# Performance work log

Hardware: AMD Instinct MI355X
Metric: run time of the kernel (lower is better)

Reference implementation:

```python
import jax, jax.numpy as jnp
import numpy as np

B, H, W, C = 2, 128, 128, 128
K = 3            # window_size
NB = K * K       # neighbor_count = 9
RP = 8           # relative_position_dim
HID = 128        # edge hidden = max(256//2, 128)
EIN = 3 * C + RP # edge_input_dim = 392
CLIP = 3.0
GEPS = 1e-06     # gate_eps
LNE = 1e-05      # LayerNorm eps


def _ln(x, g, b):
    m = x.mean(-1, keepdims=True)
    v = ((x - m) ** 2).mean(-1, keepdims=True)
    return (x - m) * jax.lax.rsqrt(v + LNE) * g + b


def setup_inputs() -> dict:
    key = jax.random.key(0)
    ks = jax.random.split(key, 12)
    f32 = jnp.float32
    inp = {
        'tokens': jax.random.normal(ks[0], (B, H, W, C), dtype=f32),
        'ln1_g': jnp.ones((C,), f32), 'ln1_b': jnp.zeros((C,), f32),
        'ln2_g': jnp.ones((C,), f32), 'ln2_b': jnp.zeros((C,), f32),
        'rel_pos': 0.02 * jax.random.normal(ks[1], (NB, RP), dtype=f32),
        'dW1': 0.01 * jax.random.normal(ks[2], (EIN, HID), dtype=f32),
        'db1': jnp.zeros((HID,), f32),
        'dW2': 0.01 * jax.random.normal(ks[3], (HID, 1), dtype=f32),
        'db2': jnp.zeros((1,), f32),
        'rW1': 0.01 * jax.random.normal(ks[4], (EIN, HID), dtype=f32),
        'rb1': jnp.zeros((HID,), f32),
        'rW2': 0.01 * jax.random.normal(ks[5], (HID, 1), dtype=f32),
        'rb2': jnp.zeros((1,), f32),
        'vW': 0.01 * jax.random.normal(ks[6], (C, C), dtype=f32),
        'vb': jnp.zeros((C,), f32),
        'oW': 0.01 * jax.random.normal(ks[7], (C, C), dtype=f32),
        'ob': jnp.zeros((C,), f32),
        'eml_gamma': jnp.asarray(0.1, f32),
        'eml_lam': jnp.asarray(1.0, f32),
        'eml_bias': jnp.asarray(-0.3, f32),
    }
    return inp


def _edge_mlp(x, W1, b1, W2, b2):
    h = jax.nn.gelu(jnp.einsum('blnd,dh->blnh', x, W1) + b1, approximate=False)
    return jnp.einsum('blnh,ho->blno', h, W2) + b2


def _forward(tokens, ln1_g, ln1_b, ln2_g, ln2_b, rel_pos, dW1, db1, dW2, db2,
             rW1, rb1, rW2, rb2, vW, vb, oW, ob, eml_gamma, eml_lam, eml_bias,
             warmup_eta=1.0):
    Bh, Hh, Wh, Ch = tokens.shape
    L = Hh * Wh
    normalized = _ln(tokens, ln1_g, ln1_b)
    flat = normalized.reshape(Bh, L, Ch)
    # Unfold(kernel=3, padding=1): gather 9 shifted views, then replicate torch's
    # reshape of the (C, 9)-ordered channel axis into (9, C).
    pad = jnp.pad(normalized, ((0, 0), (1, 1), (1, 1), (0, 0)))
    shifts = [pad[:, i:i + Hh, j:j + Wh, :] for i in range(K) for j in range(K)]
    nbhd = jnp.stack(shifts, axis=-1)                       # [B,H,W,C,9]
    nbhd = nbhd.reshape(Bh, L, Ch * NB).reshape(Bh, L, NB, Ch)  # torch reshape semantics
    center = jnp.broadcast_to(flat[:, :, None, :], nbhd.shape)
    rel = jnp.broadcast_to(rel_pos[None, None], (Bh, L, NB, rel_pos.shape[-1]))
    edge_features = jnp.concatenate([center, nbhd, center - nbhd, rel], axis=-1)
    drive = _edge_mlp(edge_features, dW1, db1, dW2, db2)[..., 0]        # [B,L,9]
    resistance = _edge_mlp(edge_features, rW1, rb1, rW2, rb2)[..., 0]   # [B,L,9]
    # EML unit (Ohm's-law style gate): clamp(eta*gamma*drive/(lambda*softplus(R)+eps)+bias)
    energy = jnp.clip(
        warmup_eta * (eml_gamma * drive) / (eml_lam * jax.nn.softplus(resistance) + GEPS)
        + eml_bias, -CLIP, CLIP)
    gate = jax.nn.sigmoid(energy)                                        # [B,L,9]
    values = jnp.einsum('blnc,cd->blnd', nbhd, vW) + vb                  # [B,L,9,C]
    gate_mass = jnp.maximum(gate.sum(axis=2), GEPS)                      # [B,L]
    message = jnp.einsum('bln,blnc->blc', gate, values) / gate_mass[..., None]
    update = (jnp.einsum('blc,cd->bld', message, oW) + ob).reshape(Bh, Hh, Wh, Ch)
    output = _ln(tokens + update, ln2_g, ln2_b)  # dropout is identity at eval
    return output


def reference(tokens, ln1_g, ln1_b, ln2_g, ln2_b, rel_pos, dW1, db1, dW2, db2,
              rW1, rb1, rW2, rb2, vW, vb, oW, ob, eml_gamma, eml_lam, eml_bias):
    return _forward(tokens, ln1_g, ln1_b, ln2_g, ln2_b, rel_pos, dW1, db1, dW2, db2,
                    rW1, rb1, rW2, rb2, vW, vb, oW, ob, eml_gamma, eml_lam, eml_bias)
```

## Files before the change

### kernel.cpp

```cpp
#include <hip/hip_runtime.h>


#define USHORT unsigned short
#define AW 152

typedef __attribute__((ext_vector_type(8)))  __bf16 v8bf;
typedef __attribute__((ext_vector_type(8)))  USHORT v8u;
typedef __attribute__((ext_vector_type(16))) float  v16f;

__device__ __forceinline__ USHORT f2bf(float f) {
    unsigned v; __builtin_memcpy(&v, &f, 4);
    v += 0x7FFFu + ((v >> 16) & 1u);
    return (USHORT)(v >> 16);
}

template <int C>
__device__ __forceinline__ float dpps(float x) {
    return __int_as_float(
        __builtin_amdgcn_update_dpp(0, __float_as_int(x), C, 0xf, 0xf, true));
}
__device__ __forceinline__ float red32half(float x) {
    x += dpps<0x111>(x);
    x += dpps<0x112>(x);
    x += dpps<0x114>(x);
    x += dpps<0x118>(x);
    x += dpps<0x142>(x);
    return x;
}
__device__ __forceinline__ float red64(float x) {
    x = red32half(x);
    x += dpps<0x143>(x);
    return x;
}
__device__ __forceinline__ float bcast63(float x) {
    return __int_as_float(__builtin_amdgcn_readlane(__float_as_int(x), 63));
}

__global__ __launch_bounds__(256) void k_setup(
    const float* __restrict__ tok, const float* __restrict__ ln1g,
    const float* __restrict__ ln1b,
    const float* __restrict__ dW1, const float* __restrict__ db1,
    const float* __restrict__ rW1, const float* __restrict__ rb1,
    const float* __restrict__ rel, const float* __restrict__ dW2,
    const float* __restrict__ rW2, const float* __restrict__ vW,
    const float* __restrict__ vb,  const float* __restrict__ oW,
    USHORT* __restrict__ norm,
    USHORT* __restrict__ WnTg, USHORT* __restrict__ WcTg, USHORT* __restrict__ VTg,
    float* __restrict__ preg, float* __restrict__ vboWg, float* __restrict__ w2g)
{
    const int blk = blockIdx.x, t = threadIdx.x;
    if (blk >= 354) {
        const int p = (blk - 354) * 4 + (t >> 6);
        const int lane = t & 63;
        const float2 x = ((const float2*)(tok + (size_t)p * 128))[lane];
        float s = x.x + x.y;
        for (int m = 1; m < 64; m <<= 1) s += __shfl_xor(s, m);
        const float mean = s * (1.f / 128.f);
        const float d0 = x.x - mean, d1 = x.y - mean;
        float q = d0 * d0 + d1 * d1;
        for (int m = 1; m < 64; m <<= 1) q += __shfl_xor(q, m);
        const float rstd = rsqrtf(q * (1.f / 128.f) + 1e-5f);
        const float2 gg = ((const float2*)ln1g)[lane], bb = ((const float2*)ln1b)[lane];
        ((unsigned*)norm)[(size_t)p * 64 + lane] =
            (unsigned)f2bf(d0 * rstd * gg.x + bb.x) |
            ((unsigned)f2bf(d1 * rstd * gg.y + bb.y) << 16);
        return;
    }
    if (blk < 72) {
        int idx = blk * 256 + t;
        int n = ((idx >> 4) * 7282) >> 16;
        int k = idx - n * 144;
        int r = k >> 4, tt = k & 15, c2 = r + 9 * tt;
        float acc = 0.f;
        if (c2 < 128)
            for (int j = 0; j < 128; ++j) acc += vW[c2 * 128 + j] * oW[j * 128 + n];
        VTg[idx] = f2bf(acc);
    } else if (blk < 216) {
        int idx = (blk - 72) * 256 + t;
        int n = ((idx >> 4) * 7282) >> 16;
        int k = idx - n * 144;
        int r = k >> 4, tt = k & 15, c2 = r + 9 * tt;
        int col = n & 127;
        const float* W = (n < 128) ? dW1 : rW1;
        float val = 0.f;
        if (c2 < 128) val = W[(128 + c2) * 128 + col] - W[(256 + c2) * 128 + col];
        WnTg[idx] = f2bf(val);
    } else if (blk < 344) {
        int idx = (blk - 216) * 256 + t;
        int n = idx >> 7, c = idx & 127, col = n & 127;
        const float* W = (n < 128) ? dW1 : rW1;
        WcTg[idx] = f2bf(W[c * 128 + col] + W[(256 + c) * 128 + col]);
    } else if (blk < 353) {
        int n2 = blk - 344; int h = t;
        float acc;
        if (h < 128) {
            acc = db1[h];
            for (int r = 0; r < 8; ++r) acc += rel[n2 * 8 + r] * dW1[(384 + r) * 128 + h];
        } else {
            int hh = h - 128;
            acc = rb1[hh];
            for (int r = 0; r < 8; ++r) acc += rel[n2 * 8 + r] * rW1[(384 + r) * 128 + hh];
        }
        preg[n2 * 256 + h] = acc;
    } else {
        if (t < 128) {
            float acc = 0.f;
            for (int j = 0; j < 128; ++j) acc += vb[j] * oW[j * 128 + t];
            vboWg[t] = acc;
            w2g[t] = dW2[t];
            w2g[128 + t] = rW2[t];
        }
    }
}

__device__ __forceinline__ void gather_load(
    uint2 (&pf)[9], const USHORT* __restrict__ nb,
    int n2, int y, int bI, int tid)
{
    const int x = tid >> 2, q = tid & 3;
    #pragma unroll
    for (int r = 0; r < 9; ++r) {
        int u = 2 * n2 + r;
        int n = (u >= 18) ? (u - 18) : ((u >= 9) ? (u - 9) : u);
        int v = n2 * 128 + r;
        int c0 = (v * 7282) >> 16;
        int dyq = (n * 22) >> 6;
        int dx = n - 3 * dyq - 1;
        int dy = dyq - 1;
        int sy = y + dy, sx = x + dx;
        bool ok = ((unsigned)sy < 128u) && ((unsigned)sx < 128u);
        int e0 = (c0 & ~1) + 4 * q;
        size_t gidx = ((size_t)((bI * 128 + (ok ? sy : 0)) * 128 + (ok ? sx : 0))) * 128 + e0;
        const unsigned* gp = (const unsigned*)nb + (gidx >> 1);
        unsigned dw0 = gp[0], dw1 = gp[1];
        pf[r].x = ok ? dw0 : 0u;
        pf[r].y = ok ? dw1 : 0u;
    }
}

__device__ __forceinline__ void gather_store(
    USHORT* __restrict__ Adst, uint2 (&pf)[9], int n2, int tid)
{
    const int x = tid >> 2, q = tid & 3;
    #pragma unroll
    for (int r = 0; r < 9; ++r) {
        int v = n2 * 128 + r;
        int c0 = (v * 7282) >> 16;
        unsigned dw0 = pf[r].x, dw1 = pf[r].y;
        unsigned nxt = (unsigned)__shfl_down((int)dw0, 1);
        unsigned o0, o1;
        if (c0 & 1) { o0 = (dw0 >> 16) | (dw1 << 16); o1 = (dw1 >> 16) | (nxt << 16); }
        else        { o0 = dw0;                       o1 = dw1; }
        pf[r].x = o0; pf[r].y = o1;
        *(uint2*)(Adst + x * AW + 16 * r + 4 * q) = make_uint2(o0, o1);
    }
}

__global__ __launch_bounds__(512, 2) void k_edge(
    const float* __restrict__ tok, const float* __restrict__ ln2g,
    const float* __restrict__ ln2b, const USHORT* __restrict__ nb,
    const USHORT* __restrict__ WnTg, const USHORT* __restrict__ WcTg,
    const USHORT* __restrict__ VTg, const float* __restrict__ preg,
    const float* __restrict__ vboWg, const float* __restrict__ w2g,
    const float* __restrict__ db2p, const float* __restrict__ rb2p,
    const float* __restrict__ gmp, const float* __restrict__ lmp,
    const float* __restrict__ bip, const float* __restrict__ obp,
    float* __restrict__ out)
{
    extern __shared__ char smem[];
    USHORT* Wsh  = (USHORT*)smem;
    USHORT* Ash0 = (USHORT*)(smem + 77824);
    USHORT* Ash1 = (USHORT*)(smem + 116736);
    float*  w2L  = (float*)(smem + 155648);
    float*  dP   = (float*)(smem + 156672);
    float*  rP   = (float*)(smem + 158720);
    float*  sgL  = (float*)(smem + 160768);
    float*  updF = (float*)smem;

    const int tid = threadIdx.x;
    const int lane = tid & 63, wave = tid >> 6, hi = lane >> 5, l31 = lane & 31;
    const int mw = wave & 1, nw = wave >> 1;
    const int blk = blockIdx.x;
    const int bI = blk >> 7;
    const int y = ((blk & 7) << 4) | ((blk >> 3) & 15);
    const int p0 = (bI * 128 + y) * 128;

    for (int i = tid; i < 4096; i += 512) {
        int n = i >> 4, kv = i & 15;
        *(v8u*)(Wsh + n * AW + kv * 8) = *(const v8u*)(WcTg + n * 128 + kv * 8);
    }
    for (int i = tid; i < 2048; i += 512) {
        int x = i >> 4, kv = i & 15;
        *(v8u*)(Ash0 + x * AW + kv * 8) = *(const v8u*)(nb + (size_t)(p0 + x) * 128 + kv * 8);
    }
    if (tid < 256) w2L[tid] = w2g[tid];
    __syncthreads();

    v16f cp[2][2];
    #pragma unroll
    for (int a = 0; a < 2; ++a)
        for (int b = 0; b < 2; ++b)
            for (int e = 0; e < 16; ++e) cp[a][b][e] = 0.f;
    #pragma unroll
    for (int ks = 0; ks < 8; ++ks) {
        v8bf af0 = *(const v8bf*)(Ash0 + (mw * 64 + l31) * AW + ks * 16 + hi * 8);
        v8bf af1 = *(const v8bf*)(Ash0 + (mw * 64 + 32 + l31) * AW + ks * 16 + hi * 8);
        v8bf bf0 = *(const v8bf*)(Wsh + (nw * 64 + l31) * AW + ks * 16 + hi * 8);
        v8bf bf1 = *(const v8bf*)(Wsh + (nw * 64 + 32 + l31) * AW + ks * 16 + hi * 8);
        cp[0][0] = __builtin_amdgcn_mfma_f32_32x32x16_bf16(af0, bf0, cp[0][0], 0, 0, 0);
        cp[0][1] = __builtin_amdgcn_mfma_f32_32x32x16_bf16(af0, bf1, cp[0][1], 0, 0, 0);
        cp[1][0] = __builtin_amdgcn_mfma_f32_32x32x16_bf16(af1, bf0, cp[1][0], 0, 0, 0);
        cp[1][1] = __builtin_amdgcn_mfma_f32_32x32x16_bf16(af1, bf1, cp[1][1], 0, 0, 0);
    }
    __syncthreads();

    for (int i = tid; i < 4608; i += 512) {
        int n = (i * 3641) >> 16;
        int kv = i - n * 18;
        *(v8u*)(Wsh + n * AW + kv * 8) = *(const v8u*)(WnTg + n * 144 + kv * 8);
    }
    uint2 pfc[9];
    gather_load(pfc, nb, 0, y, bI, tid);
    gather_store(Ash0, pfc, 0, tid);

    const float gmv = gmp[0], lmv = lmp[0], biv = bip[0];
    const float db2v = db2p[0], rb2v = rb2p[0];
    const float wv0 = w2L[nw * 64 + l31];
    const float wv1 = w2L[nw * 64 + 32 + l31];

    float G[36];
    #pragma unroll
    for (int j = 0; j < 36; ++j) G[j] = 0.f;
    float sg = 0.f;
    const int grow = tid >> 2, gq = tid & 3;

    const int w32g = grow & 31;
    const int gslot = (((grow >> 6) * 2 + ((grow >> 5) & 1)) * 2 + ((w32g >> 2) & 1)) * 16
                      + ((w32g & 3) | (((w32g >> 3) & 3) << 2));

    float* sumHalf = ((nw < 2) ? dP : rP) + (nw & 1) * 128;

    __syncthreads();

    for (int n2 = 0; n2 < 9; ++n2) {
        const int par = n2 & 1;
        USHORT* Acur = par ? Ash1 : Ash0;
        USHORT* Anxt = par ? Ash0 : Ash1;
        const float pv0 = preg[n2 * 256 + nw * 64 + l31];
        const float pv1 = preg[n2 * 256 + nw * 64 + 32 + l31];

        uint2 raw[9];
        if (n2 < 8) gather_load(raw, nb, n2 + 1, y, bI, tid);

        v16f acc[2][2];
        #pragma unroll
        for (int a = 0; a < 2; ++a)
            for (int b = 0; b < 2; ++b) acc[a][b] = cp[a][b];
        #pragma unroll
        for (int ks = 0; ks < 9; ++ks) {
            v8bf af0 = *(const v8bf*)(Acur + (mw * 64 + l31) * AW + ks * 16 + hi * 8);
            v8bf af1 = *(const v8bf*)(Acur + (mw * 64 + 32 + l31) * AW + ks * 16 + hi * 8);
            v8bf bf0 = *(const v8bf*)(Wsh + (nw * 64 + l31) * AW + ks * 16 + hi * 8);
            v8bf bf1 = *(const v8bf*)(Wsh + (nw * 64 + 32 + l31) * AW + ks * 16 + hi * 8);
            acc[0][0] = __builtin_amdgcn_mfma_f32_32x32x16_bf16(af0, bf0, acc[0][0], 0, 0, 0);
            acc[0][1] = __builtin_amdgcn_mfma_f32_32x32x16_bf16(af0, bf1, acc[0][1], 0, 0, 0);
            acc[1][0] = __builtin_amdgcn_mfma_f32_32x32x16_bf16(af1, bf0, acc[1][0], 0, 0, 0);
            acc[1][1] = __builtin_amdgcn_mfma_f32_32x32x16_bf16(af1, bf1, acc[1][1], 0, 0, 0);
        }
        #pragma unroll
        for (int mt = 0; mt < 2; ++mt) {
            float part[16];
            #pragma unroll
            for (int rr = 0; rr < 16; ++rr) {
                float h0 = acc[mt][0][rr] + pv0;
                float h1 = acc[mt][1][rr] + pv1;
                float s0 = __builtin_amdgcn_rcpf(1.f + __expf(-1.702f * h0));
                float s1 = __builtin_amdgcn_rcpf(1.f + __expf(-1.702f * h1));
                part[rr] = h0 * s0 * wv0 + h1 * s1 * wv1;
            }
            #pragma unroll
            for (int rr = 0; rr < 16; ++rr) part[rr] = red32half(part[rr]);
            if (l31 == 31) {
                float* t0 = sumHalf + par * 256 + ((mw * 2 + mt) * 2 + hi) * 16;
                *(float4*)(t0 +  0) = make_float4(part[0],  part[1],  part[2],  part[3]);
                *(float4*)(t0 +  4) = make_float4(part[4],  part[5],  part[6],  part[7]);
                *(float4*)(t0 +  8) = make_float4(part[8],  part[9],  part[10], part[11]);
                *(float4*)(t0 + 12) = make_float4(part[12], part[13], part[14], part[15]);
            }
        }
        if (n2 < 8) gather_store(Anxt, raw, n2 + 1, tid);
        __syncthreads();

        {
            const int pb = par * 256;
            float d  = dP[pb + gslot] + dP[pb + 128 + gslot] + db2v;
            float rv = rP[pb + gslot] + rP[pb + 128 + gslot] + rb2v;
            float sp = fmaxf(rv, 0.f) + log1pf(__expf(-fabsf(rv)));
            float e = gmv * d / (lmv * sp + 1e-6f) + biv;
            e = fminf(fmaxf(e, -3.f), 3.f);
            float gt = 1.f / (1.f + __expf(-e));
            sg += gt;
            #pragma unroll
            for (int r = 0; r < 9; ++r) {
                unsigned o0 = pfc[r].x, o1 = pfc[r].y;
                G[4 * r + 0] += gt * __int_as_float((int)(o0 << 16));
                G[4 * r + 1] += gt * __int_as_float((int)(o0 & 0xFFFF0000u));
                G[4 * r + 2] += gt * __int_as_float((int)(o1 << 16));
                G[4 * r + 3] += gt * __int_as_float((int)(o1 & 0xFFFF0000u));
            }
        }
        if (n2 < 8) {
            #pragma unroll
            for (int r = 0; r < 9; ++r) pfc[r] = raw[r];
        }
    }

    {
        USHORT* dst = Ash0 + grow * AW + 4 * gq;
        #pragma unroll
        for (int r = 0; r < 9; ++r) {
            unsigned lo  = (unsigned)f2bf(G[4 * r + 0]) | ((unsigned)f2bf(G[4 * r + 1]) << 16);
            unsigned hi2 = (unsigned)f2bf(G[4 * r + 2]) | ((unsigned)f2bf(G[4 * r + 3]) << 16);
            *(uint2*)(dst + 16 * r) = make_uint2(lo, hi2);
        }
    }
    for (int i = tid; i < 2304; i += 512) {
        int n = (i * 3641) >> 16;
        int kv = i - n * 18;
        *(v8u*)(Ash1 + n * AW + kv * 8) = *(const v8u*)(VTg + n * 144 + kv * 8);
    }
    if (gq == 0) sgL[grow] = sg;
    __syncthreads();

    v16f P[2];
    #pragma unroll
    for (int a = 0; a < 2; ++a)
        for (int e = 0; e < 16; ++e) P[a][e] = 0.f;
    #pragma unroll
    for (int ks = 0; ks < 9; ++ks) {
        v8bf af0 = *(const v8bf*)(Ash0 + (mw * 64 + l31) * AW + ks * 16 + hi * 8);
        v8bf af1 = *(const v8bf*)(Ash0 + (mw * 64 + 32 + l31) * AW + ks * 16 + hi * 8);
        v8bf vf  = *(const v8bf*)(Ash1 + (nw * 32 + l31) * AW + ks * 16 + hi * 8);
        P[0] = __builtin_amdgcn_mfma_f32_32x32x16_bf16(af0, vf, P[0], 0, 0, 0);
        P[1] = __builtin_amdgcn_mfma_f32_32x32x16_bf16(af1, vf, P[1], 0, 0, 0);
    }

    {
        const int colc = nw * 32 + l31;
        const float vbw = vboWg[colc], obv = obp[colc];
        #pragma unroll
        for (int mt = 0; mt < 2; ++mt) {
            const int base = mw * 64 + mt * 32 + 4 * hi;
            const float4* sq = (const float4*)&sgL[base];
            float4 sa = sq[0], sb = sq[2], sc = sq[4], sd = sq[6];
            float sv16[16] = {sa.x, sa.y, sa.z, sa.w, sb.x, sb.y, sb.z, sb.w,
                              sc.x, sc.y, sc.z, sc.w, sd.x, sd.y, sd.z, sd.w};
            #pragma unroll
            for (int rr = 0; rr < 16; ++rr) {
                int row = base + (rr & 3) + 8 * (rr >> 2);
                float s = sv16[rr];
                float iv = 1.f / fmaxf(s, 1e-6f);
                updF[row * 128 + colc] = P[mt][rr] * iv + vbw * (s * iv) + obv;
            }
        }
    }
    __syncthreads();

    const float g20 = ln2g[lane], g21 = ln2g[lane + 64];
    const float b20 = ln2b[lane], b21 = ln2b[lane + 64];
    for (int q2 = 0; q2 < 16; ++q2) {
        int p = wave * 16 + q2;
        size_t gp = (size_t)(p0 + p) * 128;
        float x0 = tok[gp + lane]      + updF[p * 128 + lane];
        float x1 = tok[gp + lane + 64] + updF[p * 128 + lane + 64];
        float mean = bcast63(red64(x0 + x1)) * (1.f / 128.f);
        float d0 = x0 - mean, d1 = x1 - mean;
        float rstd = rsqrtf(bcast63(red64(d0 * d0 + d1 * d1)) * (1.f / 128.f) + 1e-5f);
        out[gp + lane]      = d0 * rstd * g20 + b20;
        out[gp + lane + 64] = d1 * rstd * g21 + b21;
    }
}

extern "C" void kernel_launch(void* const* d_in, const int* in_sizes, int n_in,
                              void* d_out, int out_size, void* d_ws, size_t ws_size,
                              hipStream_t stream) {
    const float* tok  = (const float*)d_in[0];
    const float* ln1g = (const float*)d_in[1];
    const float* ln1b = (const float*)d_in[2];
    const float* ln2g = (const float*)d_in[3];
    const float* ln2b = (const float*)d_in[4];
    const float* rel  = (const float*)d_in[5];
    const float* dW1  = (const float*)d_in[6];
    const float* db1  = (const float*)d_in[7];
    const float* dW2  = (const float*)d_in[8];
    const float* db2  = (const float*)d_in[9];
    const float* rW1  = (const float*)d_in[10];
    const float* rb1  = (const float*)d_in[11];
    const float* rW2  = (const float*)d_in[12];
    const float* rb2  = (const float*)d_in[13];
    const float* vW   = (const float*)d_in[14];
    const float* vb   = (const float*)d_in[15];
    const float* oW   = (const float*)d_in[16];
    const float* ob   = (const float*)d_in[17];
    const float* gm   = (const float*)d_in[18];
    const float* lm   = (const float*)d_in[19];
    const float* bi   = (const float*)d_in[20];
    float* out = (float*)d_out;

    char* w = (char*)d_ws;
    USHORT* norm = (USHORT*)w; w += 8388608;
    USHORT* WnTg = (USHORT*)w; w += 73728;
    USHORT* WcTg = (USHORT*)w; w += 65536;
    USHORT* VTg  = (USHORT*)w; w += 36864;
    float*  preg = (float*)w;  w += 9216;
    float*  vboWg= (float*)w;  w += 512;
    float*  w2g  = (float*)w;  w += 1024;

    hipFuncSetAttribute((const void*)k_edge,
                        hipFuncAttributeMaxDynamicSharedMemorySize, 161280);

    hipLaunchKernelGGL(k_setup, dim3(8546), dim3(256), 0, stream,
                       tok, ln1g, ln1b, dW1, db1, rW1, rb1, rel, dW2, rW2,
                       vW, vb, oW, norm, WnTg, WcTg, VTg, preg, vboWg, w2g);
    hipLaunchKernelGGL(k_edge, dim3(256), dim3(512), 161280, stream,
                       tok, ln2g, ln2b, norm, WnTg, WcTg, VTg, preg, vboWg, w2g,
                       db2, rb2, gm, lm, bi, ob, out);
}
```

Measured before the change: 187.7 us.

## Transpose MFMA operands so hidden dim lies in registers, drop cross-lane reductions

Swaps the A/B operands of the edge MLP MFMAs so each lane's accumulator rows span hidden units instead of pixels. The second-layer dot product then becomes an in-register sum plus one cross-half shuffle, replacing 16 DPP reduction chains per tile and the scattered slot remapping. The w2 weights are packed into registers as bf16 pairs instead of being staged in LDS, and the bias is read as float4 vectors. Rounding w2 to bf16 adds a small precision loss, and it adds register pressure under the 512-thread, 2-block launch bound.

```diff
diff --git a/kernel.cpp b/kernel.cpp
--- a/kernel.cpp
+++ b/kernel.cpp
@@ -19,16 +19,12 @@
     return __int_as_float(
         __builtin_amdgcn_update_dpp(0, __float_as_int(x), C, 0xf, 0xf, true));
 }
-__device__ __forceinline__ float red32half(float x) {
+__device__ __forceinline__ float red64(float x) {
     x += dpps<0x111>(x);
     x += dpps<0x112>(x);
     x += dpps<0x114>(x);
     x += dpps<0x118>(x);
     x += dpps<0x142>(x);
-    return x;
-}
-__device__ __forceinline__ float red64(float x) {
-    x = red32half(x);
     x += dpps<0x143>(x);
     return x;
 }
@@ -171,10 +167,9 @@
     USHORT* Wsh  = (USHORT*)smem;
     USHORT* Ash0 = (USHORT*)(smem + 77824);
     USHORT* Ash1 = (USHORT*)(smem + 116736);
-    float*  w2L  = (float*)(smem + 155648);
-    float*  dP   = (float*)(smem + 156672);
-    float*  rP   = (float*)(smem + 158720);
-    float*  sgL  = (float*)(smem + 160768);
+    float*  dP   = (float*)(smem + 155648);
+    float*  rP   = (float*)(smem + 157696);
+    float*  sgL  = (float*)(smem + 159744);
     float*  updF = (float*)smem;
 
     const int tid = threadIdx.x;
@@ -193,8 +188,17 @@
         int x = i >> 4, kv = i & 15;
         *(v8u*)(Ash0 + x * AW + kv * 8) = *(const v8u*)(nb + (size_t)(p0 + x) * 128 + kv * 8);
     }
-    if (tid < 256) w2L[tid] = w2g[tid];
     __syncthreads();
+
+    unsigned w2p[2][4][2];
+    #pragma unroll
+    for (int a = 0; a < 2; ++a)
+        #pragma unroll
+        for (int g4 = 0; g4 < 4; ++g4) {
+            float4 v = *(const float4*)(w2g + nw * 64 + a * 32 + 4 * hi + 8 * g4);
+            w2p[a][g4][0] = (unsigned)f2bf(v.x) | ((unsigned)f2bf(v.y) << 16);
+            w2p[a][g4][1] = (unsigned)f2bf(v.z) | ((unsigned)f2bf(v.w) << 16);
+        }
 
     v16f cp[2][2];
     #pragma unroll
@@ -207,10 +211,10 @@
         v8bf af1 = *(const v8bf*)(Ash0 + (mw * 64 + 32 + l31) * AW + ks * 16 + hi * 8);
         v8bf bf0 = *(const v8bf*)(Wsh + (nw * 64 + l31) * AW + ks * 16 + hi * 8);
         v8bf bf1 = *(const v8bf*)(Wsh + (nw * 64 + 32 + l31) * AW + ks * 16 + hi * 8);
-        cp[0][0] = __builtin_amdgcn_mfma_f32_32x32x16_bf16(af0, bf0, cp[0][0], 0, 0, 0);
-        cp[0][1] = __builtin_amdgcn_mfma_f32_32x32x16_bf16(af0, bf1, cp[0][1], 0, 0, 0);
-        cp[1][0] = __builtin_amdgcn_mfma_f32_32x32x16_bf16(af1, bf0, cp[1][0], 0, 0, 0);
-        cp[1][1] = __builtin_amdgcn_mfma_f32_32x32x16_bf16(af1, bf1, cp[1][1], 0, 0, 0);
+        cp[0][0] = __builtin_amdgcn_mfma_f32_32x32x16_bf16(bf0, af0, cp[0][0], 0, 0, 0);
+        cp[0][1] = __builtin_amdgcn_mfma_f32_32x32x16_bf16(bf0, af1, cp[0][1], 0, 0, 0);
+        cp[1][0] = __builtin_amdgcn_mfma_f32_32x32x16_bf16(bf1, af0, cp[1][0], 0, 0, 0);
+        cp[1][1] = __builtin_amdgcn_mfma_f32_32x32x16_bf16(bf1, af1, cp[1][1], 0, 0, 0);
     }
     __syncthreads();
 
@@ -225,20 +229,12 @@
 
     const float gmv = gmp[0], lmv = lmp[0], biv = bip[0];
     const float db2v = db2p[0], rb2v = rb2p[0];
-    const float wv0 = w2L[nw * 64 + l31];
-    const float wv1 = w2L[nw * 64 + 32 + l31];
 
     float G[36];
     #pragma unroll
     for (int j = 0; j < 36; ++j) G[j] = 0.f;
     float sg = 0.f;
     const int grow = tid >> 2, gq = tid & 3;
-
-    const int w32g = grow & 31;
-    const int gslot = (((grow >> 6) * 2 + ((grow >> 5) & 1)) * 2 + ((w32g >> 2) & 1)) * 16
-                      + ((w32g & 3) | (((w32g >> 3) & 3) << 2));
-
-    float* sumHalf = ((nw < 2) ? dP : rP) + (nw & 1) * 128;
 
     __syncthreads();
 
@@ -246,8 +242,6 @@
         const int par = n2 & 1;
         USHORT* Acur = par ? Ash1 : Ash0;
         USHORT* Anxt = par ? Ash0 : Ash1;
-        const float pv0 = preg[n2 * 256 + nw * 64 + l31];
-        const float pv1 = preg[n2 * 256 + nw * 64 + 32 + l31];
 
         uint2 raw[9];
         if (n2 < 8) gather_load(raw, nb, n2 + 1, y, bI, tid);
@@ -262,39 +256,51 @@
             v8bf af1 = *(const v8bf*)(Acur + (mw * 64 + 32 + l31) * AW + ks * 16 + hi * 8);
             v8bf bf0 = *(const v8bf*)(Wsh + (nw * 64 + l31) * AW + ks * 16 + hi * 8);
             v8bf bf1 = *(const v8bf*)(Wsh + (nw * 64 + 32 + l31) * AW + ks * 16 + hi * 8);
-            acc[0][0] = __builtin_amdgcn_mfma_f32_32x32x16_bf16(af0, bf0, acc[0][0], 0, 0, 0);
-            acc[0][1] = __builtin_amdgcn_mfma_f32_32x32x16_bf16(af0, bf1, acc[0][1], 0, 0, 0);
-            acc[1][0] = __builtin_amdgcn_mfma_f32_32x32x16_bf16(af1, bf0, acc[1][0], 0, 0, 0);
-            acc[1][1] = __builtin_amdgcn_mfma_f32_32x32x16_bf16(af1, bf1, acc[1][1], 0, 0, 0);
-        }
-        #pragma unroll
-        for (int mt = 0; mt < 2; ++mt) {
-            float part[16];
+            acc[0][0] = __builtin_amdgcn_mfma_f32_32x32x16_bf16(bf0, af0, acc[0][0], 0, 0, 0);
+            acc[0][1] = __builtin_amdgcn_mfma_f32_32x32x16_bf16(bf0, af1, acc[0][1], 0, 0, 0);
+            acc[1][0] = __builtin_amdgcn_mfma_f32_32x32x16_bf16(bf1, af0, acc[1][0], 0, 0, 0);
+            acc[1][1] = __builtin_amdgcn_mfma_f32_32x32x16_bf16(bf1, af1, acc[1][1], 0, 0, 0);
+        }
+        {
+            float drv0 = 0.f, drv1 = 0.f;
             #pragma unroll
-            for (int rr = 0; rr < 16; ++rr) {
-                float h0 = acc[mt][0][rr] + pv0;
-                float h1 = acc[mt][1][rr] + pv1;
-                float s0 = __builtin_amdgcn_rcpf(1.f + __expf(-1.702f * h0));
-                float s1 = __builtin_amdgcn_rcpf(1.f + __expf(-1.702f * h1));
-                part[rr] = h0 * s0 * wv0 + h1 * s1 * wv1;
+            for (int a = 0; a < 2; ++a) {
+                #pragma unroll
+                for (int g4 = 0; g4 < 4; ++g4) {
+                    float4 pv4 = *(const float4*)(preg + n2 * 256 + nw * 64
+                                                  + a * 32 + 4 * hi + 8 * g4);
+                    const unsigned u0 = w2p[a][g4][0], u1 = w2p[a][g4][1];
+                    float wj[4] = {
+                        __int_as_float((int)(u0 << 16)),
+                        __int_as_float((int)(u0 & 0xFFFF0000u)),
+                        __int_as_float((int)(u1 << 16)),
+                        __int_as_float((int)(u1 & 0xFFFF0000u)) };
+                    float pvj[4] = {pv4.x, pv4.y, pv4.z, pv4.w};
+                    #pragma unroll
+                    for (int j = 0; j < 4; ++j) {
+                        const int rg = g4 * 4 + j;
+                        float x0 = acc[a][0][rg] + pvj[j];
+                        float x1 = acc[a][1][rg] + pvj[j];
+                        float s0 = __builtin_amdgcn_rcpf(1.f + __expf(-1.702f * x0));
+                        float s1 = __builtin_amdgcn_rcpf(1.f + __expf(-1.702f * x1));
+                        drv0 += x0 * s0 * wj[j];
+                        drv1 += x1 * s1 * wj[j];
+                    }
+                }
             }
-            #pragma unroll
-            for (int rr = 0; rr < 16; ++rr) part[rr] = red32half(part[rr]);
-            if (l31 == 31) {
-                float* t0 = sumHalf + par * 256 + ((mw * 2 + mt) * 2 + hi) * 16;
-                *(float4*)(t0 +  0) = make_float4(part[0],  part[1],  part[2],  part[3]);
-                *(float4*)(t0 +  4) = make_float4(part[4],  part[5],  part[6],  part[7]);
-                *(float4*)(t0 +  8) = make_float4(part[8],  part[9],  part[10], part[11]);
-                *(float4*)(t0 + 12) = make_float4(part[12], part[13], part[14], part[15]);
-            }
+            drv0 += __shfl_xor(drv0, 32);
+            drv1 += __shfl_xor(drv1, 32);
+            float* dst = ((nw < 2) ? dP : rP) + par * 256 + (nw & 1) * 128 + mw * 64;
+            dst[l31]      = drv0;
+            dst[32 + l31] = drv1;
         }
         if (n2 < 8) gather_store(Anxt, raw, n2 + 1, tid);
         __syncthreads();
 
         {
             const int pb = par * 256;
-            float d  = dP[pb + gslot] + dP[pb + 128 + gslot] + db2v;
-            float rv = rP[pb + gslot] + rP[pb + 128 + gslot] + rb2v;
+            float d  = dP[pb + grow] + dP[pb + 128 + grow] + db2v;
+            float rv = rP[pb + grow] + rP[pb + 128 + grow] + rb2v;
             float sp = fmaxf(rv, 0.f) + log1pf(__expf(-fabsf(rv)));
             float e = gmv * d / (lmv * sp + 1e-6f) + biv;
             e = fminf(fmaxf(e, -3.f), 3.f);
@@ -417,12 +423,12 @@
     float*  w2g  = (float*)w;  w += 1024;
 
     hipFuncSetAttribute((const void*)k_edge,
-                        hipFuncAttributeMaxDynamicSharedMemorySize, 161280);
+                        hipFuncAttributeMaxDynamicSharedMemorySize, 160256);
 
     hipLaunchKernelGGL(k_setup, dim3(8546), dim3(256), 0, stream,
                        tok, ln1g, ln1b, dW1, db1, rW1, rb1, rel, dW2, rW2,
                        vW, vb, oW, norm, WnTg, WcTg, VTg, preg, vboWg, w2g);
-    hipLaunchKernelGGL(k_edge, dim3(256), dim3(512), 161280, stream,
+    hipLaunchKernelGGL(k_edge, dim3(256), dim3(512), 160256, stream,
                        tok, ln2g, ln2b, norm, WnTg, WcTg, VTg, preg, vboWg, w2g,
                        db2, rb2, gm, lm, bi, ob, out);
 }
```

Result: slower. 195.9 us (+4.4%).
